# Kernel optimization log

Hardware: AMD Instinct MI355X
Metric: run time of the kernel (lower is better)

Reference implementation:

```python
import jax, jax.numpy as jnp
import numpy as np

EPS = 1e-5  # RMSNorm epsilon


def rmsnorm(x, w):
    return x * jax.lax.rsqrt(jnp.mean(x * x, axis=-1, keepdims=True) + EPS) * w


def mamba_forward(u, in_proj_w, conv_w, conv_b, x_proj_w, dt_proj_w, dt_proj_b,
                  A_log, D_param, mamba_out_w):
    # u: (b, L, dm) -- canonical Mamba block (expand=2, d_state=16, d_conv=4)
    b, L, dm = u.shape
    di, ds = A_log.shape
    dtr = dt_proj_w.shape[1]
    xz = jnp.einsum('bld,ed->ble', u, in_proj_w)          # (b,L,2*di)
    x_, z = jnp.split(xz, 2, axis=-1)                     # each (b,L,di)
    # causal depthwise conv over the sequence axis
    dconv = conv_w.shape[-1]
    xc = jnp.transpose(x_, (0, 2, 1))                     # (b,di,L)
    xc = jnp.pad(xc, ((0, 0), (0, 0), (dconv - 1, 0)))
    xc = jax.lax.conv_general_dilated(xc, conv_w, window_strides=(1,), padding='VALID',
                                      dimension_numbers=('NCH', 'OIH', 'NCH'),
                                      feature_group_count=di)
    xc = xc + conv_b[None, :, None]
    x_ = jax.nn.silu(jnp.transpose(xc, (0, 2, 1)))        # (b,L,di)
    # input-dependent dt, B, C
    x_dbl = jnp.einsum('bld,ed->ble', x_, x_proj_w)       # (b,L,dtr+2*ds)
    dt, B, C = jnp.split(x_dbl, [dtr, dtr + ds], axis=-1)
    delta = jax.nn.softplus(jnp.einsum('blr,dr->bld', dt, dt_proj_w) + dt_proj_b)  # (b,L,di)
    A = -jnp.exp(A_log)                                   # (di,ds)

    def step(h, inp):
        d_t, B_t, C_t, x_t = inp                          # (b,di),(b,ds),(b,ds),(b,di)
        dA = jnp.exp(d_t[:, :, None] * A)                 # (b,di,ds)
        h = dA * h + (d_t * x_t)[:, :, None] * B_t[:, None, :]
        y = jnp.einsum('bds,bs->bd', h, C_t)
        return h, y

    xs = (jnp.moveaxis(delta, 1, 0), jnp.moveaxis(B, 1, 0),
          jnp.moveaxis(C, 1, 0), jnp.moveaxis(x_, 1, 0))
    h0 = jnp.zeros((b, di, ds), dtype=u.dtype)
    _, ys = jax.lax.scan(step, h0, xs)                    # ys: (L,b,di)
    y = jnp.moveaxis(ys, 0, 1) + x_ * D_param             # (b,L,di)
    y = y * jax.nn.silu(z)
    return jnp.einsum('bld,od->blo', y, mamba_out_w)      # (b,L,dm)


def conv1x1(W, bvec, t):
    # t: (b, cin, L) -> (b, cout, L)
    return jnp.einsum('oi,bit->bot', W, t) + bvec[None, :, None]


def reference(x, w_norm1, w_norm2, W_ip, b_ip, W_fp, b_fp, W_wp, b_wp, W_op, b_op,
              in_proj_w, conv_w, conv_b, x_proj_w, dt_proj_w, dt_proj_b,
              A_log, D_param, mamba_out_w):
    # x: (b, L, D) -- module's (b, c, l) with l == input_dim = D, c == seq = L
    residual = x
    xn = rmsnorm(x, w_norm1)                 # RMSNorm over last (input_dim) axis
    xt = jnp.transpose(xn, (0, 2, 1))        # 'b c l -> b l c' : (b, D, L)
    ssm = conv1x1(W_ip, b_ip, xt)            # (b, 2D, L)
    ssm = conv1x1(W_fp, b_fp, ssm)           # (b, 2D, L)
    u = jnp.transpose(ssm, (0, 2, 1))        # (b, L, 2D): seq=L, d_model=2D
    m = mamba_forward(u, in_proj_w, conv_w, conv_b, x_proj_w, dt_proj_w, dt_proj_b,
                      A_log, D_param, mamba_out_w)
    m = rmsnorm(m, w_norm2) + u              # PostNormMamba residual
    ssm = jnp.transpose(m, (0, 2, 1))        # (b, 2D, L)
    w = conv1x1(W_wp, b_wp, xt)              # (b, 2D, L)
    w = w * jax.nn.sigmoid(w)                # swish
    out = conv1x1(W_op, b_op, w * ssm)       # (b, D, L)
    return jnp.transpose(out, (0, 2, 1)) + residual


def setup_inputs():
    key = jax.random.key(0)
    ks = jax.random.split(key, 16)
    D, L, b = 64, 4096, 4
    dm, di, ds, dconv = 2 * D, 4 * D, 16, 4
    dtr = (dm + 15) // 16  # dt_rank = ceil(d_model/16) = 8

    def n(k, shape, fan_in):
        return jax.random.normal(k, shape, jnp.float32) * (1.0 / np.sqrt(fan_in))

    return {
        'x': jax.random.normal(ks[0], (b, L, D), jnp.float32),
        'w_norm1': jnp.ones((D,), jnp.float32),
        'w_norm2': jnp.ones((dm,), jnp.float32),
        'W_ip': n(ks[1], (2 * D, D), D), 'b_ip': jnp.zeros((2 * D,), jnp.float32),
        'W_fp': n(ks[2], (2 * D, 2 * D), 2 * D), 'b_fp': jnp.zeros((2 * D,), jnp.float32),
        'W_wp': n(ks[3], (2 * D, D), D), 'b_wp': jnp.zeros((2 * D,), jnp.float32),
        'W_op': n(ks[4], (D, 2 * D), 2 * D), 'b_op': jnp.zeros((D,), jnp.float32),
        'in_proj_w': n(ks[5], (2 * di, dm), dm),
        'conv_w': n(ks[6], (di, 1, dconv), dconv),
        'conv_b': jnp.zeros((di,), jnp.float32),
        'x_proj_w': n(ks[7], (dtr + 2 * ds, di), di),
        'dt_proj_w': n(ks[8], (di, dtr), dtr),
        'dt_proj_b': jnp.full((di,), float(np.log(np.expm1(0.01))), jnp.float32),
        'A_log': jnp.log(jnp.broadcast_to(jnp.arange(1, ds + 1, dtype=jnp.float32), (di, ds))),
        'D_param': jnp.ones((di,), jnp.float32),
        'mamba_out_w': n(ks[9], (dm, di), di),
    }
```

## Files before the change

### kernel.cpp

```cpp
#include <hip/hip_runtime.h>
#include <hip/hip_bf16.h>

typedef __hip_bfloat16 bf16;
typedef __attribute__((ext_vector_type(8))) short bf16x8;
typedef __attribute__((ext_vector_type(4))) float f32x4;
#define DEV __device__ __forceinline__

constexpr int SEQ  = 4096;
constexpr int NB   = 4;
constexpr int NTOK = NB * SEQ;
constexpr float EPS = 1e-5f;
constexpr int NCH = 32;
constexpr int NCHUNK = SEQ / NCH;
constexpr float LOG2E = 1.44269504f;

constexpr int OFF_WDT  = 0;
constexpr int OFF_WB   = 2048;
constexpr int WB_IP = 0;
constexpr int WB_WP = 8192;
constexpr int WB_FP = 16384;
constexpr int WB_PR = 32768;
constexpr int WB_MO = 98304;
constexpr int WB_OP = 131072;
constexpr int WB_XP = 139264;
constexpr int WB_TOT = 151552;
constexpr int OFF_XDBL = OFF_WB + WB_TOT / 2;
constexpr int OFF_R1   = OFF_XDBL + NTOK * 40;
constexpr int OFF_WSW  = OFF_R1   + 1048576;
constexpr int OFF_U    = OFF_WSW  + 1048576;
constexpr int OFF_R2   = OFF_U    + 1048576;
constexpr int OFF_SILUZ= OFF_R2   + 2097152;
constexpr int OFF_XC   = OFF_SILUZ+ 2097152;
constexpr int OFF_G    = OFF_XC   + 2097152;
constexpr int OFF_FLAG = OFF_G    + 2097152;
constexpr int OFF_SUMM = OFF_FLAG + 16;
constexpr int OFF_HIN  = OFF_SUMM + 64 * NCHUNK * 256 * 2;

DEV float b2f(bf16 x) { return __bfloat162float(x); }
DEV bf16 f2b(float x) { return __float2bfloat16(x); }
DEV short shof(bf16 h) { short s; __builtin_memcpy(&s, &h, 2); return s; }
DEV float ldin(const void* p, int i, int f) {
  return f ? ((const float*)p)[i] : b2f(((const bf16*)p)[i]);
}
DEV unsigned pack2(float a, float b) {
  bf16 ha = f2b(a), hb = f2b(b);
  unsigned short ua, ub;
  __builtin_memcpy(&ua, &ha, 2); __builtin_memcpy(&ub, &hb, 2);
  return (unsigned)ua | ((unsigned)ub << 16);
}
DEV float lo16f(unsigned u) { return __int_as_float((int)(u << 16)); }
DEV float hi16f(unsigned u) { return __int_as_float((int)(u & 0xffff0000u)); }
template<int CTRL>
DEV float dpp_add(float v) {
  int r = __builtin_amdgcn_update_dpp(0, __float_as_int(v), CTRL, 0xF, 0xF, false);
  return v + __int_as_float(r);
}
DEV float exp2f_fast(float a) { return __builtin_amdgcn_exp2f(a); }
DEV float softplus(float a) {
  return (a > 20.f) ? a : __logf(1.f + exp2f_fast(a * LOG2E));
}
DEV float silu(float a) { return a / (1.f + __expf(-a)); }

DEV void cpw(int e, int base, int count, const void* __restrict__ src,
             bf16* __restrict__ wb, int f) {
  int r = e - base;
  if (r >= 0 && r < count) wb[base + r] = f2b(ldin(src, r, f));
}
__global__ __launch_bounds__(256) void prep_k(
    const void* __restrict__ w_ip, const void* __restrict__ w_wp, const void* __restrict__ w_fp,
    const void* __restrict__ w_pr, const void* __restrict__ w_mo, const void* __restrict__ w_op,
    const void* __restrict__ w_x,  const void* __restrict__ w_dt,
    const void* __restrict__ x, float* __restrict__ wsf, int* __restrict__ flagp)
{
  __shared__ int cnt;
  if (threadIdx.x == 0) cnt = 0;
  __syncthreads();
  {
    float v = b2f(((const bf16*)x)[threadIdx.x]);
    int ok = (v == v) && fabsf(v) > 1e-4f && fabsf(v) < 100.f;
    atomicAdd(&cnt, ok);
  }
  __syncthreads();
  int f = (cnt > 204) ? 0 : 1;
  if (blockIdx.x == 0 && threadIdx.x == 0) *flagp = f;

  int e = blockIdx.x * 256 + threadIdx.x;
  bf16* wb = (bf16*)(wsf + OFF_WB);
  cpw(e, WB_IP, 8192,  w_ip, wb, f);
  cpw(e, WB_WP, 8192,  w_wp, wb, f);
  cpw(e, WB_FP, 16384, w_fp, wb, f);
  cpw(e, WB_PR, 65536, w_pr, wb, f);
  cpw(e, WB_MO, 32768, w_mo, wb, f);
  cpw(e, WB_OP, 8192,  w_op, wb, f);
  {
    int r = e - WB_XP;
    if (r >= 0 && r < 12288) wb[WB_XP + r] = (r < 10240) ? f2b(ldin(w_x, r, f)) : f2b(0.f);
  }
  if (e < 2048) {
    int r = e >> 8, d = e & 255;
    wsf[OFF_WDT + e] = ldin(w_dt, d * 8 + r, f);
  }
}

__global__ __launch_bounds__(512) void fm_k(
    const void* __restrict__ x, const void* __restrict__ w1, const float* __restrict__ wsf,
    const void* __restrict__ b_ip, const void* __restrict__ b_wp, const void* __restrict__ b_fp,
    bf16* __restrict__ wsw, bf16* __restrict__ u, bf16* __restrict__ xpre,
    bf16* __restrict__ siluz, const int* __restrict__ flagp)
{
  __shared__ __align__(16) char smem[33280];
  short* xn   = (short*)smem;
  short* t1   = (short*)(smem + 4608);
  short* ul   = (short*)(smem + 13312);
  short* wswl = (short*)(smem + 22016);
  short* xzl  = (short*)smem;

  const int f = *flagp;
  const int tid = threadIdx.x;
  const int tok0 = blockIdx.x * 32;
  {
    const int token = tid >> 4, r = tid & 15;
    float v[4]; float ss = 0.f;
    #pragma unroll
    for (int k = 0; k < 4; ++k) {
      v[k] = ldin(x, (tok0 + token) * 64 + r * 4 + k, f);
      ss += v[k] * v[k];
    }
    ss += __shfl_xor(ss, 1, 16); ss += __shfl_xor(ss, 2, 16);
    ss += __shfl_xor(ss, 4, 16); ss += __shfl_xor(ss, 8, 16);
    float sc = rsqrtf(ss * (1.f / 64.f) + EPS);
    unsigned* dst = (unsigned*)xn + token * 36 + r * 2;
    #pragma unroll
    for (int k = 0; k < 2; ++k) {
      int i = r * 4 + k * 2;
      dst[k] = pack2(v[k*2] * sc * ldin(w1, i, f), v[k*2+1] * sc * ldin(w1, i + 1, f));
    }
  }
  __syncthreads();
  const int lane = tid & 63, m = lane & 15, q = lane >> 4;
  const int w = tid >> 6;
  {
    const int wt = w >> 2, ng = w & 3;
    const bf16* W = (const bf16*)(wsf + OFF_WB) + (wt ? WB_WP : WB_IP);
    const void* bia = wt ? b_wp : b_ip;
    bf16x8 a[2][2];
    #pragma unroll
    for (int mt = 0; mt < 2; ++mt)
      #pragma unroll
      for (int kk = 0; kk < 2; ++kk)
        a[mt][kk] = *(const bf16x8*)&xn[(mt * 16 + m) * 72 + kk * 32 + q * 8];
    #pragma unroll
    for (int nti = 0; nti < 2; ++nti) {
      int nt = ng * 2 + nti;
      int n = nt * 16 + m;
      f32x4 acc[2] = {{0,0,0,0},{0,0,0,0}};
      #pragma unroll
      for (int kk = 0; kk < 2; ++kk) {
        bf16x8 b = *(const bf16x8*)(W + (nt * 16 + m) * 64 + kk * 32 + q * 8);
        #pragma unroll
        for (int mt = 0; mt < 2; ++mt)
          acc[mt] = __builtin_amdgcn_mfma_f32_16x16x32_bf16(a[mt][kk], b, acc[mt], 0, 0, 0);
      }
      float bv = ldin(bia, n, f);
      #pragma unroll
      for (int mt = 0; mt < 2; ++mt)
        #pragma unroll
        for (int r = 0; r < 4; ++r) {
          float v = acc[mt][r] + bv;
          int row = mt * 16 + q * 4 + r;
          if (wt) wswl[row * 128 + n] = shof(f2b(silu(v)));
          else    t1[row * 136 + n] = shof(f2b(v));
        }
    }
  }
  __syncthreads();
  {
    int row = tid >> 4, c8 = (tid & 15) * 8;
    uint4 v = *(const uint4*)&wswl[row * 128 + c8];
    *(uint4*)(wsw + (tok0 + row) * 128 + c8) = v;
  }
  {
    const bf16* WF = (const bf16*)(wsf + OFF_WB) + WB_FP;
    bf16x8 a[2][4];
    #pragma unroll
    for (int mt = 0; mt < 2; ++mt)
      #pragma unroll
      for (int kk = 0; kk < 4; ++kk)
        a[mt][kk] = *(const bf16x8*)&t1[(mt * 16 + m) * 136 + kk * 32 + q * 8];
    {
      int nt = w;
      int n = nt * 16 + m;
      f32x4 acc[2] = {{0,0,0,0},{0,0,0,0}};
      #pragma unroll
      for (int kk = 0; kk < 4; ++kk) {
        bf16x8 b = *(const bf16x8*)(WF + (nt * 16 + m) * 128 + kk * 32 + q * 8);
        #pragma unroll
        for (int mt = 0; mt < 2; ++mt)
          acc[mt] = __builtin_amdgcn_mfma_f32_16x16x32_bf16(a[mt][kk], b, acc[mt], 0, 0, 0);
      }
      float bv = ldin(b_fp, n, f);
      #pragma unroll
      for (int mt = 0; mt < 2; ++mt)
        #pragma unroll
        for (int r = 0; r < 4; ++r)
          ul[(mt * 16 + q * 4 + r) * 136 + n] = shof(f2b(acc[mt][r] + bv));
    }
  }
  __syncthreads();
  {
    int row = tid >> 4, c8 = (tid & 15) * 8;
    uint4 v = *(const uint4*)&ul[row * 136 + c8];
    *(uint4*)(u + (tok0 + row) * 128 + c8) = v;
  }
  {
    const bf16* WP = (const bf16*)(wsf + OFF_WB) + WB_PR;
    bf16x8 a[2][4];
    #pragma unroll
    for (int mt = 0; mt < 2; ++mt)
      #pragma unroll
      for (int kk = 0; kk < 4; ++kk)
        a[mt][kk] = *(const bf16x8*)&ul[(mt * 16 + m) * 136 + kk * 32 + q * 8];
    __syncthreads();
    #pragma unroll
    for (int nti = 0; nti < 4; ++nti) {
      int nt = w * 4 + nti;
      int n = nt * 16 + m;
      f32x4 acc[2] = {{0,0,0,0},{0,0,0,0}};
      #pragma unroll
      for (int kk = 0; kk < 4; ++kk) {
        bf16x8 b = *(const bf16x8*)(WP + (nt * 16 + m) * 128 + kk * 32 + q * 8);
        #pragma unroll
        for (int mt = 0; mt < 2; ++mt)
          acc[mt] = __builtin_amdgcn_mfma_f32_16x16x32_bf16(a[mt][kk], b, acc[mt], 0, 0, 0);
      }
      #pragma unroll
      for (int mt = 0; mt < 2; ++mt)
        #pragma unroll
        for (int r = 0; r < 4; ++r) {
          int row = mt * 16 + q * 4 + r;
          float v = acc[mt][r];
          xzl[row * 520 + n] = shof(f2b(n < 256 ? v : silu(v)));
        }
    }
  }
  __syncthreads();
  {
    #pragma unroll
    for (int k = 0; k < 4; ++k) {
      int chunk = tid + k * 512;
      int row = chunk >> 6, seg = chunk & 63;
      uint4 v = *(const uint4*)&xzl[row * 520 + seg * 8];
      int n0 = seg * 8;
      if (n0 < 256) *(uint4*)(xpre + (tok0 + row) * 256 + n0) = v;
      else          *(uint4*)(siluz + (tok0 + row) * 256 + (n0 - 256)) = v;
    }
  }
}

__global__ __launch_bounds__(256) void conv_k(
    const bf16* __restrict__ xpre, const void* __restrict__ cw, const void* __restrict__ cb,
    const float* __restrict__ wsf, bf16* __restrict__ xc, float* __restrict__ xdbl,
    const int* __restrict__ flagp)
{
  __shared__ short xh[35 * 256];
  __shared__ short cs[32 * 264];
  const int f = *flagp;
  const int tid = threadIdx.x;
  const int tok0 = blockIdx.x * 32;
  const bool seqstart = (tok0 & (SEQ - 1)) == 0;
  for (int c = tid; c < 1120; c += 256) {
    int e0 = c * 8;
    int tt = e0 >> 8, i = e0 & 255;
    int gtok = tok0 + tt - 3;
    uint4* dst = (uint4*)(xh + e0);
    if (gtok >= 0 && !(seqstart && tt < 3)) *dst = *(const uint4*)(xpre + gtok * 256 + i);
    else                                    *dst = make_uint4(0, 0, 0, 0);
  }
  __syncthreads();
  {
    const int ch0 = (tid & 63) * 4;
    const int t0 = (tid >> 6) * 8;
    float w4[4][4], cb4[4];
    #pragma unroll
    for (int c = 0; c < 4; ++c) {
      cb4[c] = ldin(cb, ch0 + c, f);
      #pragma unroll
      for (int k = 0; k < 4; ++k) w4[c][k] = ldin(cw, (ch0 + c) * 4 + k, f);
    }
    float win[11][4];
    #pragma unroll
    for (int r = 0; r < 11; ++r) {
      uint2 v = *(const uint2*)&xh[(t0 + r) * 256 + ch0];
      win[r][0] = lo16f(v.x); win[r][1] = hi16f(v.x);
      win[r][2] = lo16f(v.y); win[r][3] = hi16f(v.y);
    }
    #pragma unroll
    for (int t = 0; t < 8; ++t) {
      unsigned pk[2];
      #pragma unroll
      for (int cp = 0; cp < 2; ++cp) {
        float o[2];
        #pragma unroll
        for (int ci = 0; ci < 2; ++ci) {
          int c = cp * 2 + ci;
          float acc = cb4[c];
          #pragma unroll
          for (int k = 0; k < 4; ++k) acc = fmaf(win[t + k][c], w4[c][k], acc);
          o[ci] = silu(acc);
        }
        pk[cp] = pack2(o[0], o[1]);
      }
      uint2 pv = make_uint2(pk[0], pk[1]);
      *(uint2*)&cs[(t0 + t) * 264 + ch0] = pv;
      *(uint2*)(xc + (tok0 + t0 + t) * 256 + ch0) = pv;
    }
  }
  __syncthreads();
  const int w = tid >> 6;
  if (w < 2) {
    const bf16* Wx = (const bf16*)(wsf + OFF_WB) + WB_XP;
    const int lane = tid & 63, m = lane & 15, quad = lane >> 4;
    f32x4 acc[3] = {{0,0,0,0},{0,0,0,0},{0,0,0,0}};
    #pragma unroll
    for (int k0 = 0; k0 < 256; k0 += 32) {
      bf16x8 af = *(const bf16x8*)&cs[(w * 16 + m) * 264 + k0 + quad * 8];
      #pragma unroll
      for (int nt = 0; nt < 3; ++nt) {
        bf16x8 bfr = *(const bf16x8*)(Wx + (nt * 16 + m) * 256 + k0 + quad * 8);
        acc[nt] = __builtin_amdgcn_mfma_f32_16x16x32_bf16(af, bfr, acc[nt], 0, 0, 0);
      }
    }
    #pragma unroll
    for (int nt = 0; nt < 3; ++nt) {
      int n = nt * 16 + m;
      if (n < 40) {
        #pragma unroll
        for (int r = 0; r < 4; ++r)
          xdbl[(tok0 + w * 16 + quad * 4 + r) * 40 + n] = acc[nt][r];
      }
    }
  }
}

template<bool IS_C>
__global__ __launch_bounds__(256) void scan_k(
    const float* __restrict__ xdbl, const bf16* __restrict__ xc, const bf16* __restrict__ siluz,
    const void* __restrict__ A_log, const void* __restrict__ D_par, const void* __restrict__ dt_b,
    const float* __restrict__ WDT, float* __restrict__ summ, const float* __restrict__ hinit,
    bf16* __restrict__ g, const int* __restrict__ flagp)
{
  const int f = *flagp;
  const int tid = threadIdx.x;
  const int bb = blockIdx.x >> 2, dgsup = blockIdx.x & 3, c = blockIdx.y;
  const int dgsub = tid >> 6, lane = tid & 63, dl = lane >> 2, squad = lane & 3;
  const int dg = dgsup * 4 + dgsub;
  const int bxOld = bb * 16 + dg;
  const int d_comp = dg * 16 + dl;
  const int bd = tid & 63;
  const int d_stg = dgsup * 64 + bd;
  const int bdc = dgsub * 16 + dl;
  const int tok_base = bb * SEQ + c * NCH;

  __shared__ float dt_l[NCH * 8];
  __shared__ float dx_l[16 * 64 * 2];
  __shared__ float Bp[16 * 16];
  __shared__ float Cp[IS_C ? 16 * 16 : 1];
  __shared__ float g_l[IS_C ? 16 * 64 : 1];

  float Aval2[4];
  #pragma unroll
  for (int j = 0; j < 4; ++j)
    Aval2[j] = -__expf(ldin(A_log, d_comp * 16 + squad * 4 + j, f)) * LOG2E;
  const float Dp_stg = ldin(D_par, d_stg, f);
  const float dtb_stg = ldin(dt_b, d_stg, f);
  float wdt[8];
  #pragma unroll
  for (int r = 0; r < 8; ++r) wdt[r] = WDT[r * 256 + d_stg];

  float h[4] = {0.f, 0.f, 0.f, 0.f};
  if (IS_C) {
    float4 hv = *(const float4*)(hinit + (bxOld * NCHUNK + c) * 256 + dl * 16 + squad * 4);
    h[0] = hv.x; h[1] = hv.y; h[2] = hv.z; h[3] = hv.w;
  }
  float sdlt = 0.f;

  if (tid < 64)
    *(float4*)(dt_l + tid * 4) = *(const float4*)(xdbl + (tok_base + (tid >> 1)) * 40 + (tid & 1) * 4);

  #pragma unroll 1
  for (int half = 0; half < 2; ++half) {
    const int tb = half * 16;
    __syncthreads();
    {
      int tl = tid >> 4, s = tid & 15;
      int tok = tok_base + tb + tl;
      Bp[tid] = xdbl[tok * 40 + 8 + s];
      if (IS_C) Cp[tid] = xdbl[tok * 40 + 24 + s];
    }
    #pragma unroll
    for (int k = 0; k < 4; ++k) {
      int tl = (tid >> 6) + k * 4;
      int tok = tok_base + tb + tl;
      const float* dtr = dt_l + (tb + tl) * 8;
      float a = dtb_stg;
      #pragma unroll
      for (int r = 0; r < 8; ++r) a = fmaf(dtr[r], wdt[r], a);
      float dlt = softplus(a);
      float xcv = b2f(xc[tok * 256 + d_stg]);
      *(float2*)(dx_l + (tl * 64 + bd) * 2) = make_float2(dlt, dlt * xcv);
    }
    __syncthreads();

    #pragma unroll 8
    for (int tl = 0; tl < 16; ++tl) {
      float2 dx = *(const float2*)(dx_l + (tl * 64 + bdc) * 2);
      float4 B4 = *(const float4*)(Bp + tl * 16 + squad * 4);
      float Bv[4] = {B4.x, B4.y, B4.z, B4.w};
      #pragma unroll
      for (int j = 0; j < 4; ++j) {
        float dA = exp2f_fast(dx.x * Aval2[j]);
        h[j] = fmaf(dA, h[j], dx.y * Bv[j]);
      }
      if (IS_C) {
        float4 C4 = *(const float4*)(Cp + tl * 16 + squad * 4);
        float p = h[0] * C4.x;
        p = fmaf(h[1], C4.y, p);
        p = fmaf(h[2], C4.z, p);
        p = fmaf(h[3], C4.w, p);
        p = dpp_add<0xB1>(p);
        p = dpp_add<0x4E>(p);
        if (squad == 0) g_l[tl * 64 + bdc] = p;
      } else {
        sdlt += dx.x;
      }
    }
    if (IS_C) {
      __syncthreads();
      #pragma unroll
      for (int k = 0; k < 4; ++k) {
        int tl = (tid >> 6) + k * 4;
        int tok = tok_base + tb + tl;
        float xcv = b2f(xc[tok * 256 + d_stg]);
        g[tok * 256 + d_stg] =
            f2b((g_l[tl * 64 + bd] + xcv * Dp_stg) * b2f(siluz[tok * 256 + d_stg]));
      }
    }
  }

  if (!IS_C) {
    float* dst = summ + ((bxOld * NCHUNK + c) * 256 + dl * 16 + squad * 4) * 2;
    *(float4*)(dst)     = make_float4(exp2f_fast(Aval2[0] * sdlt), h[0],
                                      exp2f_fast(Aval2[1] * sdlt), h[1]);
    *(float4*)(dst + 4) = make_float4(exp2f_fast(Aval2[2] * sdlt), h[2],
                                      exp2f_fast(Aval2[3] * sdlt), h[3]);
  }
}

__global__ __launch_bounds__(256) void scanB_k(const float* __restrict__ summ, float* __restrict__ hinit) {
  int bx = blockIdx.x, qq = threadIdx.x;
  float h = 0.f;
  for (int c0 = 0; c0 < NCHUNK; c0 += 16) {
    float2 sv[16];
    #pragma unroll
    for (int k = 0; k < 16; ++k)
      sv[k] = *(const float2*)(summ + ((bx * NCHUNK + c0 + k) * 256 + qq) * 2);
    #pragma unroll
    for (int k = 0; k < 16; ++k) {
      hinit[(bx * NCHUNK + c0 + k) * 256 + qq] = h;
      h = fmaf(sv[k].x, h, sv[k].y);
    }
  }
}

__global__ __launch_bounds__(512) void back_k(
    const bf16* __restrict__ g, const float* __restrict__ wsf, const void* __restrict__ w2,
    const bf16* __restrict__ u, const bf16* __restrict__ wsw, const void* __restrict__ b_op,
    const void* __restrict__ x, void* __restrict__ out, const int* __restrict__ flagp)
{
  __shared__ __align__(16) short ms[32 * 136];
  const int f = *flagp;
  const int tid = threadIdx.x;
  const int tok0 = blockIdx.x * 32;
  const int lane = tid & 63, m = lane & 15, q = lane >> 4;
  const int w = tid >> 6;
  const bf16* WM = (const bf16*)(wsf + OFF_WB) + WB_MO;
  const bf16* WO = (const bf16*)(wsf + OFF_WB) + WB_OP;
  {
    f32x4 acc[2] = {{0,0,0,0},{0,0,0,0}};
    #pragma unroll
    for (int kk = 0; kk < 8; ++kk) {
      bf16x8 a0 = *(const bf16x8*)(g + (tok0 + m) * 256 + kk * 32 + q * 8);
      bf16x8 a1 = *(const bf16x8*)(g + (tok0 + 16 + m) * 256 + kk * 32 + q * 8);
      int nt = w;
      bf16x8 b = *(const bf16x8*)(WM + (nt * 16 + m) * 256 + kk * 32 + q * 8);
      acc[0] = __builtin_amdgcn_mfma_f32_16x16x32_bf16(a0, b, acc[0], 0, 0, 0);
      acc[1] = __builtin_amdgcn_mfma_f32_16x16x32_bf16(a1, b, acc[1], 0, 0, 0);
    }
    {
      int n = w * 16 + m;
      #pragma unroll
      for (int mt = 0; mt < 2; ++mt)
        #pragma unroll
        for (int r = 0; r < 4; ++r)
          ms[(mt * 16 + q * 4 + r) * 136 + n] = shof(f2b(acc[mt][r]));
    }
  }
  __syncthreads();
  {
    const int token = tid >> 4, r = tid & 15;
    float mv[8]; float ss = 0.f;
    #pragma unroll
    for (int k = 0; k < 8; ++k) {
      mv[k] = b2f(((const bf16*)ms)[token * 136 + r * 8 + k]);
      ss += mv[k] * mv[k];
    }
    ss += __shfl_xor(ss, 1, 16); ss += __shfl_xor(ss, 2, 16);
    ss += __shfl_xor(ss, 4, 16); ss += __shfl_xor(ss, 8, 16);
    float sc = rsqrtf(ss * (1.f / 128.f) + EPS);
    #pragma unroll
    for (int k = 0; k < 8; ++k) {
      int i = r * 8 + k;
      int ga = (tok0 + token) * 128 + i;
      float v = mv[k] * sc * ldin(w2, i, f) + b2f(u[ga]);
      ms[token * 136 + i] = shof(f2b(v * b2f(wsw[ga])));
    }
  }
  __syncthreads();
  {
    const int mt = w >> 2, nt = w & 3;
    bf16x8 a[4];
    #pragma unroll
    for (int kk = 0; kk < 4; ++kk)
      a[kk] = *(const bf16x8*)&ms[(mt * 16 + m) * 136 + kk * 32 + q * 8];
    __syncthreads();
    f32x4 acc = {0,0,0,0};
    #pragma unroll
    for (int kk = 0; kk < 4; ++kk) {
      bf16x8 b = *(const bf16x8*)(WO + (nt * 16 + m) * 128 + kk * 32 + q * 8);
      acc = __builtin_amdgcn_mfma_f32_16x16x32_bf16(a[kk], b, acc, 0, 0, 0);
    }
    float* outl = (float*)ms;
    int n = nt * 16 + m;
    #pragma unroll
    for (int r = 0; r < 4; ++r)
      outl[(mt * 16 + q * 4 + r) * 68 + n] = acc[r];
  }
  __syncthreads();
  {
    const float* outl = (const float*)ms;
    int row = tid >> 4, c0 = (tid & 15) * 4;
    float v[4];
    #pragma unroll
    for (int j = 0; j < 4; ++j)
      v[j] = outl[row * 68 + c0 + j] + ldin(b_op, c0 + j, f)
           + ldin(x, (tok0 + row) * 64 + c0 + j, f);
    if (f) {
      *(float4*)((float*)out + (tok0 + row) * 64 + c0) = make_float4(v[0], v[1], v[2], v[3]);
    } else {
      uint2 pv = make_uint2(pack2(v[0], v[1]), pack2(v[2], v[3]));
      *(uint2*)((bf16*)out + (tok0 + row) * 64 + c0) = pv;
    }
  }
}

extern "C" void kernel_launch(void* const* d_in, const int* in_sizes, int n_in,
                              void* d_out, int out_size, void* d_ws, size_t ws_size,
                              hipStream_t stream) {
  (void)in_sizes; (void)n_in; (void)out_size; (void)ws_size;
  const void* x        = d_in[0];
  const void* w_norm1  = d_in[1];
  const void* w_norm2  = d_in[2];
  const void* W_ip     = d_in[3];
  const void* b_ip     = d_in[4];
  const void* W_fp     = d_in[5];
  const void* b_fp     = d_in[6];
  const void* W_wp     = d_in[7];
  const void* b_wp     = d_in[8];
  const void* W_op     = d_in[9];
  const void* b_op     = d_in[10];
  const void* in_proj  = d_in[11];
  const void* conv_w   = d_in[12];
  const void* conv_b   = d_in[13];
  const void* x_proj   = d_in[14];
  const void* dt_projw = d_in[15];
  const void* dt_projb = d_in[16];
  const void* A_log    = d_in[17];
  const void* D_par    = d_in[18];
  const void* mo_w     = d_in[19];

  float* wsf    = (float*)d_ws;
  float* xdbl   = wsf + OFF_XDBL;
  bf16*  wsw_b  = (bf16*)(wsf + OFF_WSW);
  bf16*  u_b    = (bf16*)(wsf + OFF_U);
  bf16*  xpre_b = (bf16*)(wsf + OFF_R2);
  float* summ   = wsf + OFF_SUMM;
  float* hin    = wsf + OFF_HIN;
  bf16*  siluz_b= (bf16*)(wsf + OFF_SILUZ);
  bf16*  xc_b   = (bf16*)(wsf + OFF_XC);
  bf16*  g_b    = (bf16*)(wsf + OFF_G);
  int*   flagp  = (int*)(wsf + OFF_FLAG);

  prep_k<<<dim3(592), dim3(256), 0, stream>>>(W_ip, W_wp, W_fp, in_proj, mo_w, W_op,
                                              x_proj, dt_projw, x, wsf, flagp);
  fm_k<<<dim3(NTOK / 32), dim3(512), 0, stream>>>(x, w_norm1, wsf, b_ip, b_wp, b_fp,
                                                  wsw_b, u_b, xpre_b, siluz_b, flagp);
  conv_k<<<dim3(NTOK / 32), dim3(256), 0, stream>>>(xpre_b, conv_w, conv_b, wsf, xc_b, xdbl, flagp);
  scan_k<false><<<dim3(16, NCHUNK), dim3(256), 0, stream>>>(xdbl, xc_b, siluz_b, A_log, D_par,
                                                            dt_projb, wsf + OFF_WDT, summ, hin, g_b, flagp);
  scanB_k<<<dim3(64), dim3(256), 0, stream>>>(summ, hin);
  scan_k<true><<<dim3(16, NCHUNK), dim3(256), 0, stream>>>(xdbl, xc_b, siluz_b, A_log, D_par,
                                                           dt_projb, wsf + OFF_WDT, summ, hin, g_b, flagp);
  back_k<<<dim3(NTOK / 32), dim3(512), 0, stream>>>(g_b, wsf, w_norm2, u_b, wsw_b, b_op, x, d_out, flagp);
}
```

Measured before the change: 197.9 us.

## Split chunked scan into local pass plus closed-form carry correction

The first scan pass now also emits per-token local outputs (C·h_local) and cumulative delta sums into fp32 buffers. The correction pass then adds the carried-in state's contribution in closed form, C·exp(A·cumdelta)·h_in, instead of rerunning the full recurrence with its delta, softplus and B loads. This shortens the serial dependency chain in the second pass. In exchange it adds about 32 MB of fp32 writes and reads for ploc and cumd, plus extra exp2 work.

```diff
diff --git a/kernel.cpp b/kernel.cpp
--- a/kernel.cpp
+++ b/kernel.cpp
@@ -35,6 +35,8 @@
 constexpr int OFF_FLAG = OFF_G    + 2097152;
 constexpr int OFF_SUMM = OFF_FLAG + 16;
 constexpr int OFF_HIN  = OFF_SUMM + 64 * NCHUNK * 256 * 2;
+constexpr int OFF_PLOC = OFF_HIN  + 64 * NCHUNK * 256;
+constexpr int OFF_CUMD = OFF_PLOC + NTOK * 256;
 
 DEV float b2f(bf16 x) { return __bfloat162float(x); }
 DEV bf16 f2b(float x) { return __float2bfloat16(x); }
@@ -342,12 +344,11 @@
   }
 }
 
-template<bool IS_C>
-__global__ __launch_bounds__(256) void scan_k(
-    const float* __restrict__ xdbl, const bf16* __restrict__ xc, const bf16* __restrict__ siluz,
-    const void* __restrict__ A_log, const void* __restrict__ D_par, const void* __restrict__ dt_b,
-    const float* __restrict__ WDT, float* __restrict__ summ, const float* __restrict__ hinit,
-    bf16* __restrict__ g, const int* __restrict__ flagp)
+__global__ __launch_bounds__(256) void scanF_k(
+    const float* __restrict__ xdbl, const bf16* __restrict__ xc,
+    const void* __restrict__ A_log, const void* __restrict__ dt_b,
+    const float* __restrict__ WDT, float* __restrict__ summ,
+    float* __restrict__ ploc, float* __restrict__ cumd, const int* __restrict__ flagp)
 {
   const int f = *flagp;
   const int tid = threadIdx.x;
@@ -364,24 +365,20 @@
   __shared__ float dt_l[NCH * 8];
   __shared__ float dx_l[16 * 64 * 2];
   __shared__ float Bp[16 * 16];
-  __shared__ float Cp[IS_C ? 16 * 16 : 1];
-  __shared__ float g_l[IS_C ? 16 * 64 : 1];
+  __shared__ float Cp[16 * 16];
+  __shared__ float pg_l[16 * 64];
+  __shared__ float cd_l[16 * 64];
 
   float Aval2[4];
   #pragma unroll
   for (int j = 0; j < 4; ++j)
     Aval2[j] = -__expf(ldin(A_log, d_comp * 16 + squad * 4 + j, f)) * LOG2E;
-  const float Dp_stg = ldin(D_par, d_stg, f);
   const float dtb_stg = ldin(dt_b, d_stg, f);
   float wdt[8];
   #pragma unroll
   for (int r = 0; r < 8; ++r) wdt[r] = WDT[r * 256 + d_stg];
 
   float h[4] = {0.f, 0.f, 0.f, 0.f};
-  if (IS_C) {
-    float4 hv = *(const float4*)(hinit + (bxOld * NCHUNK + c) * 256 + dl * 16 + squad * 4);
-    h[0] = hv.x; h[1] = hv.y; h[2] = hv.z; h[3] = hv.w;
-  }
   float sdlt = 0.f;
 
   if (tid < 64)
@@ -395,7 +392,7 @@
       int tl = tid >> 4, s = tid & 15;
       int tok = tok_base + tb + tl;
       Bp[tid] = xdbl[tok * 40 + 8 + s];
-      if (IS_C) Cp[tid] = xdbl[tok * 40 + 24 + s];
+      Cp[tid] = xdbl[tok * 40 + 24 + s];
     }
     #pragma unroll
     for (int k = 0; k < 4; ++k) {
@@ -421,39 +418,31 @@
         float dA = exp2f_fast(dx.x * Aval2[j]);
         h[j] = fmaf(dA, h[j], dx.y * Bv[j]);
       }
-      if (IS_C) {
-        float4 C4 = *(const float4*)(Cp + tl * 16 + squad * 4);
-        float p = h[0] * C4.x;
-        p = fmaf(h[1], C4.y, p);
-        p = fmaf(h[2], C4.z, p);
-        p = fmaf(h[3], C4.w, p);
-        p = dpp_add<0xB1>(p);
-        p = dpp_add<0x4E>(p);
-        if (squad == 0) g_l[tl * 64 + bdc] = p;
-      } else {
-        sdlt += dx.x;
-      }
-    }
-    if (IS_C) {
-      __syncthreads();
-      #pragma unroll
-      for (int k = 0; k < 4; ++k) {
-        int tl = (tid >> 6) + k * 4;
-        int tok = tok_base + tb + tl;
-        float xcv = b2f(xc[tok * 256 + d_stg]);
-        g[tok * 256 + d_stg] =
-            f2b((g_l[tl * 64 + bd] + xcv * Dp_stg) * b2f(siluz[tok * 256 + d_stg]));
-      }
-    }
-  }
-
-  if (!IS_C) {
-    float* dst = summ + ((bxOld * NCHUNK + c) * 256 + dl * 16 + squad * 4) * 2;
-    *(float4*)(dst)     = make_float4(exp2f_fast(Aval2[0] * sdlt), h[0],
-                                      exp2f_fast(Aval2[1] * sdlt), h[1]);
-    *(float4*)(dst + 4) = make_float4(exp2f_fast(Aval2[2] * sdlt), h[2],
-                                      exp2f_fast(Aval2[3] * sdlt), h[3]);
-  }
+      sdlt += dx.x;
+      float4 C4 = *(const float4*)(Cp + tl * 16 + squad * 4);
+      float p = h[0] * C4.x;
+      p = fmaf(h[1], C4.y, p);
+      p = fmaf(h[2], C4.z, p);
+      p = fmaf(h[3], C4.w, p);
+      p = dpp_add<0xB1>(p);
+      p = dpp_add<0x4E>(p);
+      if (squad == 0) { pg_l[tl * 64 + bdc] = p; cd_l[tl * 64 + bdc] = sdlt; }
+    }
+    __syncthreads();
+    #pragma unroll
+    for (int k = 0; k < 4; ++k) {
+      int tl = (tid >> 6) + k * 4;
+      int tok = tok_base + tb + tl;
+      ploc[tok * 256 + d_stg] = pg_l[tl * 64 + bd];
+      cumd[tok * 256 + d_stg] = cd_l[tl * 64 + bd];
+    }
+  }
+
+  float* dst = summ + ((bxOld * NCHUNK + c) * 256 + dl * 16 + squad * 4) * 2;
+  *(float4*)(dst)     = make_float4(exp2f_fast(Aval2[0] * sdlt), h[0],
+                                    exp2f_fast(Aval2[1] * sdlt), h[1]);
+  *(float4*)(dst + 4) = make_float4(exp2f_fast(Aval2[2] * sdlt), h[2],
+                                    exp2f_fast(Aval2[3] * sdlt), h[3]);
 }
 
 __global__ __launch_bounds__(256) void scanB_k(const float* __restrict__ summ, float* __restrict__ hinit) {
@@ -469,6 +458,73 @@
       hinit[(bx * NCHUNK + c0 + k) * 256 + qq] = h;
       h = fmaf(sv[k].x, h, sv[k].y);
     }
+  }
+}
+
+__global__ __launch_bounds__(256) void scanC_k(
+    const float* __restrict__ xdbl, const bf16* __restrict__ xc, const bf16* __restrict__ siluz,
+    const void* __restrict__ A_log, const void* __restrict__ D_par,
+    const float* __restrict__ hinit, const float* __restrict__ ploc,
+    const float* __restrict__ cumd, bf16* __restrict__ g, const int* __restrict__ flagp)
+{
+  const int f = *flagp;
+  const int tid = threadIdx.x;
+  const int bb = blockIdx.x >> 2, dgsup = blockIdx.x & 3, c = blockIdx.y;
+  const int dgsub = tid >> 6, lane = tid & 63, dl = lane >> 2, squad = lane & 3;
+  const int dg = dgsup * 4 + dgsub;
+  const int bxOld = bb * 16 + dg;
+  const int d_comp = dg * 16 + dl;
+  const int bd = tid & 63;
+  const int d_stg = dgsup * 64 + bd;
+  const int bdc = dgsub * 16 + dl;
+  const int tok_base = bb * SEQ + c * NCH;
+
+  __shared__ float Cp[NCH * 16];
+  __shared__ float cd_l[NCH * 64];
+  __shared__ float g_l[NCH * 64];
+
+  float Aval2[4];
+  #pragma unroll
+  for (int j = 0; j < 4; ++j)
+    Aval2[j] = -__expf(ldin(A_log, d_comp * 16 + squad * 4 + j, f)) * LOG2E;
+  const float Dp_stg = ldin(D_par, d_stg, f);
+
+  float4 hv = *(const float4*)(hinit + (bxOld * NCHUNK + c) * 256 + dl * 16 + squad * 4);
+
+  #pragma unroll
+  for (int k = 0; k < 2; ++k) {
+    int e = tid + k * 256;
+    int tl = e >> 4, s = e & 15;
+    Cp[e] = xdbl[(tok_base + tl) * 40 + 24 + s];
+  }
+  #pragma unroll
+  for (int k = 0; k < 8; ++k) {
+    int tl = (tid >> 6) + k * 4;
+    cd_l[tl * 64 + bd] = cumd[(tok_base + tl) * 256 + d_stg];
+  }
+  __syncthreads();
+
+  #pragma unroll 8
+  for (int tl = 0; tl < NCH; ++tl) {
+    float cum = cd_l[tl * 64 + bdc];
+    float4 C4 = *(const float4*)(Cp + tl * 16 + squad * 4);
+    float p =      C4.x * exp2f_fast(cum * Aval2[0]) * hv.x;
+    p = fmaf(C4.y * exp2f_fast(cum * Aval2[1]), hv.y, p);
+    p = fmaf(C4.z * exp2f_fast(cum * Aval2[2]), hv.z, p);
+    p = fmaf(C4.w * exp2f_fast(cum * Aval2[3]), hv.w, p);
+    p = dpp_add<0xB1>(p);
+    p = dpp_add<0x4E>(p);
+    if (squad == 0) g_l[tl * 64 + bdc] = p;
+  }
+  __syncthreads();
+
+  #pragma unroll
+  for (int k = 0; k < 8; ++k) {
+    int tl = (tid >> 6) + k * 4;
+    int tok = tok_base + tl;
+    float pf = ploc[tok * 256 + d_stg] + g_l[tl * 64 + bd];
+    float xcv = b2f(xc[tok * 256 + d_stg]);
+    g[tok * 256 + d_stg] = f2b((pf + xcv * Dp_stg) * b2f(siluz[tok * 256 + d_stg]));
   }
 }
 
@@ -595,6 +651,8 @@
   bf16*  xpre_b = (bf16*)(wsf + OFF_R2);
   float* summ   = wsf + OFF_SUMM;
   float* hin    = wsf + OFF_HIN;
+  float* plocp  = wsf + OFF_PLOC;
+  float* cumdp  = wsf + OFF_CUMD;
   bf16*  siluz_b= (bf16*)(wsf + OFF_SILUZ);
   bf16*  xc_b   = (bf16*)(wsf + OFF_XC);
   bf16*  g_b    = (bf16*)(wsf + OFF_G);
@@ -605,10 +663,10 @@
   fm_k<<<dim3(NTOK / 32), dim3(512), 0, stream>>>(x, w_norm1, wsf, b_ip, b_wp, b_fp,
                                                   wsw_b, u_b, xpre_b, siluz_b, flagp);
   conv_k<<<dim3(NTOK / 32), dim3(256), 0, stream>>>(xpre_b, conv_w, conv_b, wsf, xc_b, xdbl, flagp);
-  scan_k<false><<<dim3(16, NCHUNK), dim3(256), 0, stream>>>(xdbl, xc_b, siluz_b, A_log, D_par,
-                                                            dt_projb, wsf + OFF_WDT, summ, hin, g_b, flagp);
+  scanF_k<<<dim3(16, NCHUNK), dim3(256), 0, stream>>>(xdbl, xc_b, A_log, dt_projb,
+                                                      wsf + OFF_WDT, summ, plocp, cumdp, flagp);
   scanB_k<<<dim3(64), dim3(256), 0, stream>>>(summ, hin);
-  scan_k<true><<<dim3(16, NCHUNK), dim3(256), 0, stream>>>(xdbl, xc_b, siluz_b, A_log, D_par,
-                                                           dt_projb, wsf + OFF_WDT, summ, hin, g_b, flagp);
+  scanC_k<<<dim3(16, NCHUNK), dim3(256), 0, stream>>>(xdbl, xc_b, siluz_b, A_log, D_par,
+                                                      hin, plocp, cumdp, g_b, flagp);
   back_k<<<dim3(NTOK / 32), dim3(512), 0, stream>>>(g_b, wsf, w_norm2, u_b, wsw_b, b_op, x, d_out, flagp);
 }
```

Measured after the change: 198.4 us. About the same (+0.3%).
